# Performance work log

Hardware: AMD Instinct MI355X
Metric: run time of the kernel (lower is better)

Reference implementation:

```python
import jax, jax.numpy as jnp
import numpy as np

LAMBDA = 0.5
ALPHA_PRE = 1.0
ALPHA_DA = 1.0

B, N, C, T, O = 8, 1024, 64, 12, 64


def setup_inputs() -> dict:
    key = jax.random.key(0)
    ks = jax.random.split(key, 10)
    s = 0.1  # keep tanh out of deep saturation, like xavier-init scales
    return {
        "x": jax.random.normal(ks[0], (B, N, C, T), dtype=jnp.float32),
        "static_adj": jax.random.uniform(ks[1], (N, N), dtype=jnp.float32) / N,
        "W0": jax.random.normal(ks[2], (C, O), dtype=jnp.float32) * s,
        "b0": jax.random.normal(ks[3], (O,), dtype=jnp.float32) * s,
        "Ws": jax.random.normal(ks[4], (T, C, O), dtype=jnp.float32) * s,
        "bs": jax.random.normal(ks[5], (T, O), dtype=jnp.float32) * s,
        "Wd": jax.random.normal(ks[6], (T, C, O), dtype=jnp.float32) * s,
        "bd": jax.random.normal(ks[7], (T, O), dtype=jnp.float32) * s,
        "E1": jax.random.normal(ks[8], (T, N, O), dtype=jnp.float32) * s,
        "E2": jax.random.normal(ks[9], (T, N, O), dtype=jnp.float32) * s,
    }


def reference(x, static_adj, W0, b0, Ws, bs, Wd, bd, E1, E2):
    # x: [B,N,C,T] -> [T,B,N,C] so the per-timestep layers vectorize over leading T.
    xt = jnp.transpose(x, (3, 0, 1, 2))  # [T,B,N,C]
    n = xt.shape[2]

    # shared top-level linear
    x0 = jnp.einsum('tbnc,co->tbno', xt, W0) + b0  # [T,B,N,O]

    # static GCN per timestep: linear(static_adj @ x_t)
    sagg = jnp.einsum('nm,tbmc->tbnc', static_adj, xt)
    static_out = jnp.einsum('tbnc,tco->tbno', sagg, Ws) + bs[:, None, None, :]

    # dynamic GCN: base = linear_t(x_t)
    base = jnp.einsum('tbnc,tco->tbno', xt, Wd) + bd[:, None, None, :]
    DE1 = jnp.tanh(ALPHA_PRE * (base * E1[:, None]))  # [T,B,N,O]
    DE2 = jnp.tanh(ALPHA_PRE * (base * E2[:, None]))
    # cross = DE1@DE2^T - DE2@DE1^T = M - M^T
    M = jnp.einsum('tbno,tbmo->tbnm', DE1, DE2)  # [T,B,N,N]
    DA = jax.nn.relu(jnp.tanh(ALPHA_DA * (M - jnp.swapaxes(M, -1, -2))))

    # symmetric degree normalization of (DA + I)
    DA = DA + jnp.eye(n, dtype=DA.dtype)
    rowsum = jnp.clip(DA.sum(axis=-1), 1e-12, None)
    d_inv_sqrt = rowsum ** -0.5
    DA = DA * d_inv_sqrt[..., :, None] * d_inv_sqrt[..., None, :]

    dagg = jnp.einsum('tbnm,tbmc->tbnc', DA, xt)
    dyn_out = jnp.einsum('tbnc,tco->tbno', dagg, Wd) + bd[:, None, None, :]

    fused = (LAMBDA - 0.025) * static_out + (1.0 - LAMBDA - 0.025) * dyn_out + 0.05 * x0
    return jnp.transpose(fused, (1, 2, 3, 0))  # [B,N,O,T]
```

## Files before the change

### kernel.cpp

```cpp
#include <hip/hip_runtime.h>

#define BB 8
#define NN 1024
#define CC 64
#define TT 12
#define OO 64

typedef unsigned short u16;
typedef __attribute__((ext_vector_type(8))) short s16x8;
typedef __attribute__((ext_vector_type(4))) float f32x4;
typedef __attribute__((ext_vector_type(4))) unsigned int u32x4;
typedef __attribute__((ext_vector_type(2))) unsigned int u32x2;

__device__ __forceinline__ u16 f2bu(float f){
  union { float f; unsigned u; } v; v.f = f;
  unsigned r = v.u + 0x7FFFu + ((v.u >> 16) & 1u);
  return (u16)(r >> 16);
}
__device__ __forceinline__ float b2f(u16 h){
  union { unsigned u; float f; } v; v.u = ((unsigned)h) << 16; return v.f;
}
__device__ __forceinline__ float relu_tanh(float d){
  float e = __expf(2.0f * d);
  return fmaxf(1.0f - 2.0f * __builtin_amdgcn_rcpf(e + 1.0f), 0.0f);
}
__device__ __forceinline__ float tanh_fast(float d){
  float e = __expf(2.0f * d);
  return 1.0f - 2.0f * __builtin_amdgcn_rcpf(e + 1.0f);
}
__device__ __forceinline__ float tanh_sgn(float x){
  float ax = fabsf(x);
  float e = __expf(2.0f * ax);
  float t = 1.0f - 2.0f * __builtin_amdgcn_rcpf(e + 1.0f);
  return x < 0.0f ? -t : t;
}

#define MFMA16(a,b,c) __builtin_amdgcn_mfma_f32_16x16x32_bf16((a),(b),(c),0,0,0)

__device__ __forceinline__ s16x8 ld72(const u16* s, int row0, int ko, int lane){
  return *(const s16x8*)(s + (row0 + (lane & 15)) * 72 + ko + ((lane >> 4) << 3));
}

__global__ __launch_bounds__(256) void k0_transpose(const float* __restrict__ x,
                                                    u16* __restrict__ xt){
  const int n = blockIdx.x, b = blockIdx.y;
  __shared__ float s[CC*TT];
  const float* src = x + (size_t)(b*NN + n)*CC*TT;
  for (int k = threadIdx.x; k < CC*TT; k += 256) s[k] = src[k];
  __syncthreads();
  for (int k = threadIdx.x; k < CC*TT; k += 256){
    const int t = k >> 6, c = k & 63;
    xt[(((size_t)t*BB + b)*NN + n)*CC + c] = f2bu(s[c*TT + t]);
  }
}

__global__ __launch_bounds__(256) void kadj(const float* __restrict__ adj,
                                            u16* __restrict__ adjb){
  const size_t i = ((size_t)blockIdx.x*256 + threadIdx.x)*4;
  const float4 v = *(const float4*)(adj + i);
  u16 o0=f2bu(v.x), o1=f2bu(v.y), o2=f2bu(v.z), o3=f2bu(v.w);
  adjb[i]=o0; adjb[i+1]=o1; adjb[i+2]=o2; adjb[i+3]=o3;
}

__global__ __launch_bounds__(256) void kinit(float* __restrict__ rs){
  const size_t i = (size_t)blockIdx.x*256 + threadIdx.x;
  if (i < (size_t)TT*BB*NN) rs[i] = 1.0f;
}

__global__ __launch_bounds__(256) void k1_de(const u16* __restrict__ xt,
    const float* __restrict__ Wd, const float* __restrict__ bd,
    const float* __restrict__ E1, const float* __restrict__ E2,
    u16* __restrict__ DE1g, u16* __restrict__ DE2g){
  __shared__ __align__(16) u16 sWd[64*72];
  const int tid = threadIdx.x, lane = tid & 63, wid = tid >> 6;
  const int l15 = lane & 15, lr4 = lane >> 4;
  const int it = blockIdx.x, b = blockIdx.y, t = blockIdx.z;
  const int n0 = it * 64;
  for (int k = tid; k < 4096; k += 256){
    const int o = k & 63, c = k >> 6;
    sWd[o*72 + c] = f2bu(Wd[(size_t)t*4096 + c*64 + o]);
  }
  __syncthreads();
  const size_t tb = (size_t)t*BB + b;
  const u16* gx = xt + (tb*NN + n0)*CC;
  const int wrow = wid * 16;
  const f32x4 fz = {0.f,0.f,0.f,0.f};
  f32x4 acc[4] = {fz, fz, fz, fz};
  #pragma unroll
  for (int ks = 0; ks < 2; ++ks){
    const int ko = ks*32;
    const s16x8 a = *(const s16x8*)(gx + (wrow + l15)*CC + ko + (lr4 << 3));
    #pragma unroll
    for (int v = 0; v < 4; ++v)
      acc[v] = MFMA16(a, ld72(sWd, v*16, ko, lane), acc[v]);
  }
  #pragma unroll
  for (int v = 0; v < 4; ++v){
    const int o = v*16 + l15;
    const float bdv = bd[t*OO + o];
    #pragma unroll
    for (int e = 0; e < 4; ++e){
      const int n = n0 + wrow + (lr4 << 2) + e;
      const float base = acc[v][e] + bdv;
      const size_t eo = ((size_t)t*NN + n)*OO + o;
      const size_t so = (tb*NN + n)*OO + o;
      DE1g[so] = f2bu(tanh_sgn(base * E1[eo]));
      DE2g[so] = f2bu(tanh_sgn(base * E2[eo]));
    }
  }
}

__global__ __launch_bounds__(256) void k2a(const u16* __restrict__ DE1g,
    const u16* __restrict__ DE2g, float* __restrict__ rowsum){
  __shared__ __align__(16) u16 s1A[64*72], s2nA[64*72];
  __shared__ __align__(16) u16 s1B[64*72], s2nB[64*72];
  const int tid = threadIdx.x, lane = tid & 63, wid = tid >> 6;
  const int l15 = lane & 15, lr4 = lane >> 4;
  const int nwg = 8*BB*TT;
  const int logical = ((int)blockIdx.x & 7)*(nwg >> 3) + ((int)blockIdx.x >> 3);
  const int p = logical & 7;
  const size_t tb = (size_t)(logical >> 3);
  const int tiA = p, tiB = 15 - p;
  const u16* g1 = DE1g + tb*NN*OO;
  const u16* g2 = DE2g + tb*NN*OO;
  for (int k = tid; k < 512; k += 256){
    const int r = k >> 3, c = (k & 7) << 3;
    *(s16x8*)(s1A + r*72 + c) = *(const s16x8*)(g1 + (size_t)(tiA*64 + r)*OO + c);
    s16x8 vA = *(const s16x8*)(g2 + (size_t)(tiA*64 + r)*OO + c);
    u32x4 wA = *(u32x4*)&vA; wA ^= 0x80008000u;
    *(u32x4*)(s2nA + r*72 + c) = wA;
    *(s16x8*)(s1B + r*72 + c) = *(const s16x8*)(g1 + (size_t)(tiB*64 + r)*OO + c);
    s16x8 vB = *(const s16x8*)(g2 + (size_t)(tiB*64 + r)*OO + c);
    u32x4 wB = *(u32x4*)&vB; wB ^= 0x80008000u;
    *(u32x4*)(s2nB + r*72 + c) = wB;
  }
  __syncthreads();
  const int wrow = wid * 16;
  s16x8 a1A[2], na2A[2], a1B[2], na2B[2];
  #pragma unroll
  for (int ks = 0; ks < 2; ++ks){
    a1A[ks]  = ld72(s1A,  wrow, ks*32, lane);
    na2A[ks] = ld72(s2nA, wrow, ks*32, lane);
    a1B[ks]  = ld72(s1B,  wrow, ks*32, lane);
    na2B[ks] = ld72(s2nB, wrow, ks*32, lane);
  }
  u16* sJ1 = s1A;
  u16* sJ2 = s2nA;
  const int srow = tid >> 2, sc0 = (tid & 3) << 4;
  s16x8 pB1a,pB1b, pB2a,pB2b;
#define LOADT(TJ) do { \
    pB1a = *(const s16x8*)(g2 + (size_t)((TJ)*64 + srow)*OO + sc0); \
    pB1b = *(const s16x8*)(g2 + (size_t)((TJ)*64 + srow)*OO + sc0 + 8); \
    pB2a = *(const s16x8*)(g1 + (size_t)((TJ)*64 + srow)*OO + sc0); \
    pB2b = *(const s16x8*)(g1 + (size_t)((TJ)*64 + srow)*OO + sc0 + 8); \
  } while (0)
  LOADT(p);
  float rpA[4] = {0.f,0.f,0.f,0.f}, rpB[4] = {0.f,0.f,0.f,0.f};
  const f32x4 fz = {0.f,0.f,0.f,0.f};
  float* rsg = rowsum + tb*NN;
  __syncthreads();
  for (int tj = p; tj < 16; ++tj){
    *(s16x8*)(sJ1 + srow*72 + sc0)     = pB1a;
    *(s16x8*)(sJ1 + srow*72 + sc0 + 8) = pB1b;
    *(s16x8*)(sJ2 + srow*72 + sc0)     = pB2a;
    *(s16x8*)(sJ2 + srow*72 + sc0 + 8) = pB2b;
    __syncthreads();
    if (tj < 15) LOADT(tj + 1);
    s16x8 b1[4], b2[4], b1h[4], b2h[4];
    #pragma unroll
    for (int v = 0; v < 4; ++v){
      b1[v]  = ld72(sJ1, v*16, 0,  lane);
      b2[v]  = ld72(sJ2, v*16, 0,  lane);
      b1h[v] = ld72(sJ1, v*16, 32, lane);
      b2h[v] = ld72(sJ2, v*16, 32, lane);
    }
    {
      f32x4 z[4];
      #pragma unroll
      for (int v = 0; v < 4; ++v){
        z[v] = MFMA16(a1A[0],  b1[v],  fz);
        z[v] = MFMA16(na2A[0], b2[v],  z[v]);
        z[v] = MFMA16(a1A[1],  b1h[v], z[v]);
        z[v] = MFMA16(na2A[1], b2h[v], z[v]);
      }
      float colp[4] = {0.f,0.f,0.f,0.f};
      #pragma unroll
      for (int v = 0; v < 4; ++v)
        #pragma unroll
        for (int e = 0; e < 4; ++e){
          const float th = tanh_fast(z[v][e]);
          rpA[e]  += fmaxf(th, 0.f);
          colp[v] += fmaxf(-th, 0.f);
        }
      if (tj > tiA){
        #pragma unroll
        for (int v = 0; v < 4; ++v){
          float c = colp[v];
          c += __shfl_xor(c, 16); c += __shfl_xor(c, 32);
          if (lane < 16) atomicAdd(&rsg[tj*64 + v*16 + lane], c);
        }
      }
    }
    if (tj >= tiB){
      f32x4 z[4];
      #pragma unroll
      for (int v = 0; v < 4; ++v){
        z[v] = MFMA16(a1B[0],  b1[v],  fz);
        z[v] = MFMA16(na2B[0], b2[v],  z[v]);
        z[v] = MFMA16(a1B[1],  b1h[v], z[v]);
        z[v] = MFMA16(na2B[1], b2h[v], z[v]);
      }
      float colp[4] = {0.f,0.f,0.f,0.f};
      #pragma unroll
      for (int v = 0; v < 4; ++v)
        #pragma unroll
        for (int e = 0; e < 4; ++e){
          const float th = tanh_fast(z[v][e]);
          rpB[e]  += fmaxf(th, 0.f);
          colp[v] += fmaxf(-th, 0.f);
        }
      if (tj > tiB){
        #pragma unroll
        for (int v = 0; v < 4; ++v){
          float c = colp[v];
          c += __shfl_xor(c, 16); c += __shfl_xor(c, 32);
          if (lane < 16) atomicAdd(&rsg[tj*64 + v*16 + lane], c);
        }
      }
    }
    __syncthreads();
  }
#undef LOADT
  #pragma unroll
  for (int e = 0; e < 4; ++e){
    float r = rpA[e];
    r += __shfl_xor(r, 1); r += __shfl_xor(r, 2);
    r += __shfl_xor(r, 4); r += __shfl_xor(r, 8);
    if (l15 == 0) atomicAdd(&rsg[tiA*64 + wrow + (lr4 << 2) + e], r);
  }
  #pragma unroll
  for (int e = 0; e < 4; ++e){
    float r = rpB[e];
    r += __shfl_xor(r, 1); r += __shfl_xor(r, 2);
    r += __shfl_xor(r, 4); r += __shfl_xor(r, 8);
    if (l15 == 0) atomicAdd(&rsg[tiB*64 + wrow + (lr4 << 2) + e], r);
  }
}

__global__ __launch_bounds__(256) void k3b(const u16* __restrict__ xt,
    const float* __restrict__ Wd, const float* __restrict__ Ws,
    const float* __restrict__ W0, const float* __restrict__ bd,
    const float* __restrict__ bs, const float* __restrict__ b0,
    const float* __restrict__ rowsum, u16* __restrict__ xdvT,
    u16* __restrict__ xswT, u16* __restrict__ x0w){
  __shared__ __align__(16) u16 sW[64*72];
  const int tid = threadIdx.x, lane = tid & 63, wid = tid >> 6;
  const int l15 = lane & 15, lr4 = lane >> 4;
  const int it = blockIdx.x, b = blockIdx.y, t = blockIdx.z;
  const size_t tb = (size_t)t*BB + b;
  const int n0 = it * 128, wrow = wid * 32;
  const float* dvb = rowsum + tb*NN + n0;
  float dis[2][4];
  #pragma unroll
  for (int u = 0; u < 2; ++u)
    #pragma unroll
    for (int e = 0; e < 4; ++e)
      dis[u][e] = rsqrtf(dvb[wrow + u*16 + (lr4 << 2) + e]);
  float badd[4];
  #pragma unroll
  for (int v = 0; v < 4; ++v){
    const int o = v*16 + l15;
    badd[v] = 0.475f*(bd[t*OO + o] + bs[t*OO + o]) + 0.05f*b0[o];
  }
  const u16* gx = xt + (tb*NN + n0)*CC;
  const f32x4 fz = {0.f,0.f,0.f,0.f};
  for (int pass = 0; pass < 3; ++pass){
    __syncthreads();
    {
      const float* Wsrc = (pass == 0) ? (Wd + (size_t)t*4096)
                        : (pass == 1) ? (Ws + (size_t)t*4096) : W0;
      const float scale = (pass == 2) ? 0.05f : 0.475f;
      for (int k = tid; k < 4096; k += 256){
        const int o = k & 63, c = k >> 6;
        sW[o*72 + c] = f2bu(scale * Wsrc[c*64 + o]);
      }
    }
    __syncthreads();
    f32x4 acc[2][4];
    #pragma unroll
    for (int u = 0; u < 2; ++u)
      #pragma unroll
      for (int v = 0; v < 4; ++v) acc[u][v] = fz;
    #pragma unroll
    for (int ks = 0; ks < 2; ++ks){
      const int ko = ks*32;
      s16x8 bw[4];
      #pragma unroll
      for (int v = 0; v < 4; ++v) bw[v] = ld72(sW, v*16, ko, lane);
      #pragma unroll
      for (int u = 0; u < 2; ++u){
        const s16x8 a = *(const s16x8*)(gx + (wrow + u*16 + l15)*CC + ko + (lr4 << 3));
        #pragma unroll
        for (int v = 0; v < 4; ++v) acc[u][v] = MFMA16(a, bw[v], acc[u][v]);
      }
    }
    #pragma unroll
    for (int u = 0; u < 2; ++u)
      #pragma unroll
      for (int v = 0; v < 4; ++v){
        const int o = v*16 + l15;
        #pragma unroll
        for (int e = 0; e < 4; ++e){
          const int nl = wrow + u*16 + (lr4 << 2) + e;
          float val = acc[u][v][e];
          if (pass == 0)      xdvT[(tb*OO + o)*NN + n0 + nl] = f2bu(val * dis[u][e]);
          else if (pass == 1) xswT[(tb*OO + o)*NN + n0 + nl] = f2bu(val);
          else                x0w[(tb*NN + n0 + nl)*OO + o]  = f2bu(val + badd[v]);
        }
      }
  }
}

__global__ __launch_bounds__(256) void k4s(const u16* __restrict__ adjb,
    const u16* __restrict__ xswT, u16* __restrict__ outSta){
  __shared__ __align__(16) u16 sJ[64*72], sS[64*72];
  const int tid = threadIdx.x, lane = tid & 63, wid = tid >> 6;
  const int l15 = lane & 15, lr4 = lane >> 4;
  const int nwg = 16*BB*TT;
  const int logical = ((int)blockIdx.x & 7)*(nwg >> 3) + ((int)blockIdx.x >> 3);
  const int ti = logical / (BB*TT);
  const size_t tb = (size_t)(logical % (BB*TT));
  const u16* xs = xswT + tb*OO*NN;
  const int i0 = ti * 64, wrow = wid * 16;
  const int srow = tid >> 2, sc0 = (tid & 3) << 4;
  s16x8 pJa, pJb, pSa, pSb;
#define LOADS(TJ) do { \
    pJa = *(const s16x8*)(adjb + (size_t)(i0 + srow)*NN + (TJ)*64 + sc0); \
    pJb = *(const s16x8*)(adjb + (size_t)(i0 + srow)*NN + (TJ)*64 + sc0 + 8); \
    pSa = *(const s16x8*)(xs   + (size_t)srow*NN + (TJ)*64 + sc0); \
    pSb = *(const s16x8*)(xs   + (size_t)srow*NN + (TJ)*64 + sc0 + 8); \
  } while (0)
  LOADS(0);
  const f32x4 fz = {0.f,0.f,0.f,0.f};
  f32x4 as_[4] = {fz,fz,fz,fz};
  for (int tj = 0; tj < 16; ++tj){
    *(s16x8*)(sJ + srow*72 + sc0)     = pJa;
    *(s16x8*)(sJ + srow*72 + sc0 + 8) = pJb;
    *(s16x8*)(sS + srow*72 + sc0)     = pSa;
    *(s16x8*)(sS + srow*72 + sc0 + 8) = pSb;
    __syncthreads();
    if (tj < 15) LOADS(tj + 1);
    const s16x8 aJ0 = ld72(sJ, wrow, 0,  lane);
    const s16x8 aJ1 = ld72(sJ, wrow, 32, lane);
    #pragma unroll
    for (int v = 0; v < 4; ++v){
      as_[v] = MFMA16(aJ0, ld72(sS, v*16, 0,  lane), as_[v]);
      as_[v] = MFMA16(aJ1, ld72(sS, v*16, 32, lane), as_[v]);
    }
    __syncthreads();
  }
#undef LOADS
  #pragma unroll
  for (int v = 0; v < 4; ++v){
    const int o = v*16 + l15;
    #pragma unroll
    for (int e = 0; e < 4; ++e){
      const int n = i0 + wrow + (lr4 << 2) + e;
      outSta[(tb*NN + n)*OO + o] = f2bu(as_[v][e]);
    }
  }
}

__global__ __launch_bounds__(256) void k2bf(const u16* __restrict__ DE1g,
    const u16* __restrict__ DE2g, const u16* __restrict__ xdvT,
    const float* __restrict__ rowsum, float* __restrict__ outT){
  __shared__ __align__(16) u16 sB1[64*72], sB2[64*72], sXD[64*72];
  __shared__ __align__(16) u16 bounce[4][16*72];
  const int tid = threadIdx.x, lane = tid & 63, wid = tid >> 6;
  const int l15 = lane & 15, lr4 = lane >> 4;
  const int nwg = 16*BB*TT;
  const int logical = ((int)blockIdx.x & 7)*(nwg >> 3) + ((int)blockIdx.x >> 3);
  const int ti = logical & 15;
  const size_t tb = (size_t)(logical >> 4);
  const u16* g1 = DE1g + tb*NN*OO;
  const u16* g2 = DE2g + tb*NN*OO;
  const u16* xd = xdvT + tb*OO*NN;
  const float* dv = rowsum + tb*NN;
  const int i0 = ti * 64;
  for (int k = tid; k < 512; k += 256){
    const int r = k >> 3, c = (k & 7) << 3;
    *(s16x8*)(sB1 + r*72 + c) = *(const s16x8*)(g1 + (size_t)(i0 + r)*OO + c);
    s16x8 v = *(const s16x8*)(g2 + (size_t)(i0 + r)*OO + c);
    u32x4 w = *(u32x4*)&v; w ^= 0x80008000u;
    *(u32x4*)(sB2 + r*72 + c) = w;
  }
  __syncthreads();
  const int wrow = wid * 16;
  s16x8 a1[2], na2[2];
  #pragma unroll
  for (int ks = 0; ks < 2; ++ks){
    a1[ks]  = ld72(sB1, wrow, ks*32, lane);
    na2[ks] = ld72(sB2, wrow, ks*32, lane);
  }
  const int srow = tid >> 2, sc0 = (tid & 3) << 4;
  s16x8 pB1a,pB1b, pB2a,pB2b, pXDa,pXDb;
#define LOADT(TJ) do { \
    pB1a = *(const s16x8*)(g2 + (size_t)((TJ)*64 + srow)*OO + sc0); \
    pB1b = *(const s16x8*)(g2 + (size_t)((TJ)*64 + srow)*OO + sc0 + 8); \
    pB2a = *(const s16x8*)(g1 + (size_t)((TJ)*64 + srow)*OO + sc0); \
    pB2b = *(const s16x8*)(g1 + (size_t)((TJ)*64 + srow)*OO + sc0 + 8); \
    pXDa = *(const s16x8*)(xd + (size_t)srow*NN + (TJ)*64 + sc0); \
    pXDb = *(const s16x8*)(xd + (size_t)srow*NN + (TJ)*64 + sc0 + 8); \
  } while (0)
  LOADT(0);
  unsigned* wb32 = (unsigned*)bounce[wid];
  u16* wb = bounce[wid];
  const f32x4 fz = {0.f,0.f,0.f,0.f};
  f32x4 ad[4] = {fz,fz,fz,fz};
  __syncthreads();
  for (int tj = 0; tj < 16; ++tj){
    *(s16x8*)(sB1 + srow*72 + sc0)     = pB1a;
    *(s16x8*)(sB1 + srow*72 + sc0 + 8) = pB1b;
    *(s16x8*)(sB2 + srow*72 + sc0)     = pB2a;
    *(s16x8*)(sB2 + srow*72 + sc0 + 8) = pB2b;
    *(s16x8*)(sXD + srow*72 + sc0)     = pXDa;
    *(s16x8*)(sXD + srow*72 + sc0 + 8) = pXDb;
    __syncthreads();
    if (tj < 15) LOADT(tj + 1);
    f32x4 y[4];
    #pragma unroll
    for (int v = 0; v < 4; ++v){
      y[v] = MFMA16(ld72(sB1, v*16, 0,  lane), a1[0],  fz);
      y[v] = MFMA16(ld72(sB2, v*16, 0,  lane), na2[0], y[v]);
      y[v] = MFMA16(ld72(sB1, v*16, 32, lane), a1[1],  y[v]);
      y[v] = MFMA16(ld72(sB2, v*16, 32, lane), na2[1], y[v]);
    }
    #pragma unroll
    for (int v = 0; v < 4; ++v){
      const float q0 = relu_tanh(y[v][0]), q1 = relu_tanh(y[v][1]);
      const float q2 = relu_tanh(y[v][2]), q3 = relu_tanh(y[v][3]);
      unsigned w0, w1;
      asm("v_cvt_pk_bf16_f32 %0, %1, %2" : "=v"(w0) : "v"(q0), "v"(q1));
      asm("v_cvt_pk_bf16_f32 %0, %1, %2" : "=v"(w1) : "v"(q2), "v"(q3));
      u32x2 pk; pk[0] = w0; pk[1] = w1;
      *(u32x2*)(wb32 + l15*36 + v*8 + (lr4 << 1)) = pk;
    }
    asm volatile("s_waitcnt lgkmcnt(0)" ::: "memory");
    __builtin_amdgcn_sched_barrier(0);
    s16x8 pa0 = ld72(wb, 0, 0,  lane);
    s16x8 pa1 = ld72(wb, 0, 32, lane);
    #pragma unroll
    for (int v = 0; v < 4; ++v){
      ad[v] = MFMA16(pa0, ld72(sXD, v*16, 0,  lane), ad[v]);
      ad[v] = MFMA16(pa1, ld72(sXD, v*16, 32, lane), ad[v]);
    }
    __syncthreads();
  }
#undef LOADT
  const int grow0 = i0 + wrow + (lr4 << 2);
  float disv[4];
  #pragma unroll
  for (int e = 0; e < 4; ++e) disv[e] = rsqrtf(dv[grow0 + e]);
  #pragma unroll
  for (int v = 0; v < 4; ++v){
    const int o = v*16 + l15;
    #pragma unroll
    for (int e = 0; e < 4; ++e){
      const float xw = b2f(xd[(size_t)o*NN + grow0 + e]);
      outT[(tb*NN + grow0 + e)*OO + o] = disv[e]*(ad[v][e] + xw);
    }
  }
}

__global__ __launch_bounds__(256) void k5(const float* __restrict__ outT,
                                          const u16* __restrict__ x0w,
                                          const u16* __restrict__ outSta,
                                          float* __restrict__ out){
  __shared__ float s[16*64*12];
  const int tid = threadIdx.x;
  const int nb = blockIdx.x, b = blockIdx.y;
  const int n0 = nb * 16;
  for (int t = 0; t < TT; ++t){
    for (int k = tid; k < 1024; k += 256){
      const int r = k >> 6, o = k & 63;
      const size_t idx = (((size_t)t*BB + b)*NN + n0 + r)*OO + o;
      s[(r*64 + o)*12 + t] = outT[idx] + b2f(x0w[idx]) + b2f(outSta[idx]);
    }
  }
  __syncthreads();
  float* dst = out + (size_t)(b*NN + n0)*OO*TT;
  for (int k = tid; k < 16*64*12; k += 256) dst[k] = s[k];
}

extern "C" void kernel_launch(void* const* d_in, const int* in_sizes, int n_in,
                              void* d_out, int out_size, void* d_ws, size_t ws_size,
                              hipStream_t stream) {
  const float* x   = (const float*)d_in[0];
  const float* adj = (const float*)d_in[1];
  const float* W0  = (const float*)d_in[2];
  const float* b0  = (const float*)d_in[3];
  const float* Ws  = (const float*)d_in[4];
  const float* bs  = (const float*)d_in[5];
  const float* Wd  = (const float*)d_in[6];
  const float* bd  = (const float*)d_in[7];
  const float* E1  = (const float*)d_in[8];
  const float* E2  = (const float*)d_in[9];
  float* out = (float*)d_out;

  char* w = (char*)d_ws;
  size_t off = 0;
  auto take = [&](size_t bytes) -> char* {
    char* p = w + off;
    off += bytes; off = (off + 255) & ~(size_t)255;
    return p;
  };
  const size_t NE = (size_t)TT*BB*NN*OO;
  u16*   xt    = (u16*)  take(NE*2);
  u16*   adjb  = (u16*)  take((size_t)NN*NN*2);
  u16*   DE1   = (u16*)  take(NE*2);
  u16*   DE2   = (u16*)  take(NE*2);
  float* rowsum= (float*)take((size_t)TT*BB*NN*4);
  u16*   xdvT  = (u16*)  take(NE*2);
  u16*   xswT  = (u16*)  take(NE*2);
  u16*   x0w   = (u16*)  take(NE*2);
  u16*   outSta= (u16*)  take(NE*2);
  float* outT  = (float*)take(NE*4);

  k0_transpose<<<dim3(NN, BB), 256, 0, stream>>>(x, xt);
  kadj<<<dim3((NN*NN)/1024), 256, 0, stream>>>(adj, adjb);
  kinit<<<dim3((TT*BB*NN + 255)/256), 256, 0, stream>>>(rowsum);
  k1_de<<<dim3(16, BB, TT), 256, 0, stream>>>(xt, Wd, bd, E1, E2, DE1, DE2);
  k2a<<<dim3(8*BB*TT), 256, 0, stream>>>(DE1, DE2, rowsum);
  k3b<<<dim3(8, BB, TT), 256, 0, stream>>>(xt, Wd, Ws, W0, bd, bs, b0,
                                           rowsum, xdvT, xswT, x0w);
  k4s<<<dim3(16*BB*TT), 256, 0, stream>>>(adjb, xswT, outSta);
  k2bf<<<dim3(16*BB*TT), 256, 0, stream>>>(DE1, DE2, xdvT, rowsum, outT);
  k5<<<dim3(NN/16, BB), 256, 0, stream>>>(outT, x0w, outSta, out);
}
```

Before: 226.7 us.

## Eliminate LDS bounce by permuting xd k-order to match MFMA output layout

Removes the per-wave shared-memory bounce buffer used to transpose the relu-tanh adjacency tile from MFMA accumulator layout into A-operand layout. The MFMA output registers are instead packed directly into the A operand. To keep the K dimension consistent, the xd tile is written into LDS with a permuted column order (kap mapping) using 8-byte stores. This saves LDS writes, a waitcnt and reads per tile, at the cost of narrower scattered LDS stores and possible bank conflicts.

```diff
diff --git a/kernel.cpp b/kernel.cpp
--- a/kernel.cpp
+++ b/kernel.cpp
@@ -375,7 +375,6 @@
     const u16* __restrict__ DE2g, const u16* __restrict__ xdvT,
     const float* __restrict__ rowsum, float* __restrict__ outT){
   __shared__ __align__(16) u16 sB1[64*72], sB2[64*72], sXD[64*72];
-  __shared__ __align__(16) u16 bounce[4][16*72];
   const int tid = threadIdx.x, lane = tid & 63, wid = tid >> 6;
   const int l15 = lane & 15, lr4 = lane >> 4;
   const int nwg = 16*BB*TT;
@@ -403,6 +402,13 @@
     na2[ks] = ld72(sB2, wrow, ks*32, lane);
   }
   const int srow = tid >> 2, sc0 = (tid & 3) << 4;
+  const int g0 = sc0 >> 2;
+  int kap[4];
+  #pragma unroll
+  for (int q = 0; q < 4; ++q){
+    const int g = g0 + q;
+    kap[q] = ((g & 3) << 3) + (((g >> 2) & 1) << 2) + ((g >> 3) << 5);
+  }
   s16x8 pB1a,pB1b, pB2a,pB2b, pXDa,pXDb;
 #define LOADT(TJ) do { \
     pB1a = *(const s16x8*)(g2 + (size_t)((TJ)*64 + srow)*OO + sc0); \
@@ -413,8 +419,6 @@
     pXDb = *(const s16x8*)(xd + (size_t)srow*NN + (TJ)*64 + sc0 + 8); \
   } while (0)
   LOADT(0);
-  unsigned* wb32 = (unsigned*)bounce[wid];
-  u16* wb = bounce[wid];
   const f32x4 fz = {0.f,0.f,0.f,0.f};
   f32x4 ad[4] = {fz,fz,fz,fz};
   __syncthreads();
@@ -423,8 +427,19 @@
     *(s16x8*)(sB1 + srow*72 + sc0 + 8) = pB1b;
     *(s16x8*)(sB2 + srow*72 + sc0)     = pB2a;
     *(s16x8*)(sB2 + srow*72 + sc0 + 8) = pB2b;
-    *(s16x8*)(sXD + srow*72 + sc0)     = pXDa;
-    *(s16x8*)(sXD + srow*72 + sc0 + 8) = pXDb;
+    {
+      const u32x4 xa = *(const u32x4*)&pXDa;
+      const u32x4 xb = *(const u32x4*)&pXDb;
+      u32x2 h;
+      h[0] = xa[0]; h[1] = xa[1];
+      *(u32x2*)(sXD + srow*72 + kap[0]) = h;
+      h[0] = xa[2]; h[1] = xa[3];
+      *(u32x2*)(sXD + srow*72 + kap[1]) = h;
+      h[0] = xb[0]; h[1] = xb[1];
+      *(u32x2*)(sXD + srow*72 + kap[2]) = h;
+      h[0] = xb[2]; h[1] = xb[3];
+      *(u32x2*)(sXD + srow*72 + kap[3]) = h;
+    }
     __syncthreads();
     if (tj < 15) LOADT(tj + 1);
     f32x4 y[4];
@@ -435,20 +450,23 @@
       y[v] = MFMA16(ld72(sB1, v*16, 32, lane), a1[1],  y[v]);
       y[v] = MFMA16(ld72(sB2, v*16, 32, lane), na2[1], y[v]);
     }
-    #pragma unroll
-    for (int v = 0; v < 4; ++v){
-      const float q0 = relu_tanh(y[v][0]), q1 = relu_tanh(y[v][1]);
-      const float q2 = relu_tanh(y[v][2]), q3 = relu_tanh(y[v][3]);
-      unsigned w0, w1;
-      asm("v_cvt_pk_bf16_f32 %0, %1, %2" : "=v"(w0) : "v"(q0), "v"(q1));
-      asm("v_cvt_pk_bf16_f32 %0, %1, %2" : "=v"(w1) : "v"(q2), "v"(q3));
-      u32x2 pk; pk[0] = w0; pk[1] = w1;
-      *(u32x2*)(wb32 + l15*36 + v*8 + (lr4 << 1)) = pk;
-    }
-    asm volatile("s_waitcnt lgkmcnt(0)" ::: "memory");
-    __builtin_amdgcn_sched_barrier(0);
-    s16x8 pa0 = ld72(wb, 0, 0,  lane);
-    s16x8 pa1 = ld72(wb, 0, 32, lane);
+    float q[4][4];
+    #pragma unroll
+    for (int v = 0; v < 4; ++v)
+      #pragma unroll
+      for (int e = 0; e < 4; ++e)
+        q[v][e] = relu_tanh(y[v][e]);
+    u32x4 w0, w1;
+    asm("v_cvt_pk_bf16_f32 %0, %1, %2" : "=v"(w0[0]) : "v"(q[0][0]), "v"(q[0][1]));
+    asm("v_cvt_pk_bf16_f32 %0, %1, %2" : "=v"(w0[1]) : "v"(q[0][2]), "v"(q[0][3]));
+    asm("v_cvt_pk_bf16_f32 %0, %1, %2" : "=v"(w0[2]) : "v"(q[1][0]), "v"(q[1][1]));
+    asm("v_cvt_pk_bf16_f32 %0, %1, %2" : "=v"(w0[3]) : "v"(q[1][2]), "v"(q[1][3]));
+    asm("v_cvt_pk_bf16_f32 %0, %1, %2" : "=v"(w1[0]) : "v"(q[2][0]), "v"(q[2][1]));
+    asm("v_cvt_pk_bf16_f32 %0, %1, %2" : "=v"(w1[1]) : "v"(q[2][2]), "v"(q[2][3]));
+    asm("v_cvt_pk_bf16_f32 %0, %1, %2" : "=v"(w1[2]) : "v"(q[3][0]), "v"(q[3][1]));
+    asm("v_cvt_pk_bf16_f32 %0, %1, %2" : "=v"(w1[3]) : "v"(q[3][2]), "v"(q[3][3]));
+    const s16x8 pa0 = *(const s16x8*)&w0;
+    const s16x8 pa1 = *(const s16x8*)&w1;
     #pragma unroll
     for (int v = 0; v < 4; ++v){
       ad[v] = MFMA16(pa0, ld72(sXD, v*16, 0,  lane), ad[v]);
```

Measured after the change: 219.7 us. -3.1%, faster.
